# Kernel tuning notes

Hardware: AMD Instinct MI355X
Metric: run time of the kernel (lower is better)

Reference implementation:

```python
import jax, jax.numpy as jnp
import numpy as np

B, N, C = 4, 4096, 1024
H, W = 16, 256
D = C // H  # 64 head_dim


def _rope(t, f):
    # t: (B, N, H, D), f: (N, D//2, 2) -> pairwise rotation on consecutive channel pairs
    tr = t.reshape(*t.shape[:-1], D // 2, 2)
    fc = f.reshape(1, N, 1, D // 2, 2)
    out = jnp.stack([
        tr[..., 0] * fc[..., 0] - tr[..., 1] * fc[..., 1],
        tr[..., 1] * fc[..., 0] + tr[..., 0] * fc[..., 1],
    ], axis=-1)
    return out.reshape(t.shape)


def setup_inputs() -> dict:
    key = jax.random.key(0)
    ks = jax.random.split(key, 4)
    x = jax.random.normal(ks[0], (B, N, C), dtype=jnp.float32)
    freqs_cis = jax.random.normal(ks[1], (N, D // 2, 2), dtype=jnp.float32)
    qkv_w = jax.random.normal(ks[2], (3 * C, C), dtype=jnp.float32) * (C ** -0.5)
    proj_w = jax.random.normal(ks[3], (C, C), dtype=jnp.float32) * (C ** -0.5)
    proj_b = jnp.zeros((C,), dtype=jnp.float32)
    return {"x": x, "freqs_cis": freqs_cis, "qkv_w": qkv_w, "proj_w": proj_w, "proj_b": proj_b}


def reference(x, freqs_cis, qkv_w, proj_w, proj_b):
    nW = N // W
    scale = D ** -0.5
    qkv = (x @ qkv_w.T).reshape(B, N, 3, H, D)
    q, k, v = qkv[:, :, 0], qkv[:, :, 1], qkv[:, :, 2]  # (B, N, H, D)
    q = _rope(q, freqs_cis)
    k = _rope(k, freqs_cis)
    # block-diagonal window attention: q_idx//W == kv_idx//W
    qw = q.transpose(0, 2, 1, 3).reshape(B, H, nW, W, D)
    kw = k.transpose(0, 2, 1, 3).reshape(B, H, nW, W, D)
    vw = v.transpose(0, 2, 1, 3).reshape(B, H, nW, W, D)
    scores = jnp.einsum('bhwqd,bhwkd->bhwqk', qw, kw) * scale
    attn = jax.nn.softmax(scores, axis=-1)
    out = jnp.einsum('bhwqk,bhwkd->bhwqd', attn, vw)
    out = out.reshape(B, H, N, D).transpose(0, 2, 1, 3).reshape(B, N, C)
    return out @ proj_w.T + proj_b
```

## Files before the change

### kernel.cpp

```cpp
#include <hip/hip_runtime.h>
#include <stdint.h>
#include <stddef.h>

typedef __bf16 bf16;
typedef __bf16 bf16x4 __attribute__((ext_vector_type(4)));
typedef __bf16 bf16x8 __attribute__((ext_vector_type(8)));
typedef float f32x4 __attribute__((ext_vector_type(4)));

#define MFMA(a, b, c) __builtin_amdgcn_mfma_f32_16x16x32_bf16(a, b, c, 0, 0, 0)

static constexpr int kB = 4, kN = 4096, kC = 1024, kH = 16, kD = 64;
static constexpr int kM = kB * kN;
static constexpr int kK = 1024;
static constexpr int kQKVN = 3072;

__device__ __forceinline__ void cp16(const void* g, void* l) {
  __builtin_amdgcn_global_load_lds(
      (const __attribute__((address_space(1))) void*)g,
      (__attribute__((address_space(3))) void*)l, 16, 0, 0);
}

__global__ __launch_bounds__(256) void cvt_bf16(const float* __restrict__ src,
                                                bf16* __restrict__ dst, int n4) {
  const int i = blockIdx.x * 256 + threadIdx.x;
  if (i < n4) {
    const float4 v = ((const float4*)src)[i];
    bf16x4 o = {(bf16)v.x, (bf16)v.y, (bf16)v.z, (bf16)v.w};
    *(bf16x4*)&dst[4 * i] = o;
  }
}

__device__ __forceinline__ bf16x8 rope8(bf16x8 t, bf16x8 f) {
  bf16x8 o;
#pragma unroll
  for (int p = 0; p < 4; ++p) {
    float t0 = (float)t[2 * p], t1 = (float)t[2 * p + 1];
    float f0 = (float)f[2 * p], f1 = (float)f[2 * p + 1];
    o[2 * p]     = (bf16)(t0 * f0 - t1 * f1);
    o[2 * p + 1] = (bf16)(t1 * f0 + t0 * f1);
  }
  return o;
}

template <int NOUT, bool BIAS, typename OutT>
__global__ __launch_bounds__(512, 2) void gemm_bt(const bf16* __restrict__ A,
                                                  const bf16* __restrict__ Bw,
                                                  const float* __restrict__ bias,
                                                  OutT* __restrict__ Cout) {
  __shared__ unsigned short As[4][256 * 32];
  __shared__ unsigned short Bs[4][256 * 32];
  const int tid = threadIdx.x;
  const int wave = tid >> 6, lane = tid & 63;
  const int q4 = lane >> 4, l16 = lane & 15;
  const int wr = wave >> 2, wc = wave & 3;

  const int nwg = gridDim.x * gridDim.y;
  int bid = blockIdx.y * gridDim.x + blockIdx.x;
  bid = (bid & 7) * (nwg >> 3) + (bid >> 3);
  const int bx = bid % gridDim.x, by = bid / gridDim.x;
  const int n0 = bx * 256, m0 = by * 256;

  constexpr int NT = kK / 32;

  f32x4 acc[8][4] = {};

  auto stageA = [&](int kt) {
    const int buf = kt & 3;
#pragma unroll
    for (int i = 0; i < 2; ++i) {
      const int c = i * 512 + tid;
      const int row = c >> 2, s = c & 3;
      const int kb = s ^ ((row >> 1) & 3);
      cp16(A + (size_t)(m0 + row) * kK + kt * 32 + kb * 8, &As[buf][c * 8]);
    }
  };
  auto stageB = [&](int kt) {
    const int buf = kt & 3;
#pragma unroll
    for (int i = 0; i < 2; ++i) {
      const int c = i * 512 + tid;
      const int row = c >> 2, s = c & 3;
      const int kb = s ^ ((row >> 1) & 3);
      cp16(Bw + (size_t)(n0 + row) * kK + kt * 32 + kb * 8, &Bs[buf][c * 8]);
    }
  };

  stageA(0); stageB(0); stageA(1); stageB(1); stageA(2); stageB(2);
  asm volatile("s_waitcnt vmcnt(8)\n\ts_barrier" ::: "memory");

  const int slot8 = (q4 ^ ((l16 >> 1) & 3)) * 8;
  const int arow = wr * 128 + l16;
  const int bcol = wc * 64 + l16;

  for (int t = 0; t < NT; ++t) {
    const int rb = t & 3;
    bf16x8 a[8], b0, b1;
#pragma unroll
    for (int i = 0; i < 8; ++i)
      a[i] = *(const bf16x8*)&As[rb][(arow + i * 16) * 32 + slot8];
    b0 = *(const bf16x8*)&Bs[rb][bcol * 32 + slot8];
    b1 = *(const bf16x8*)&Bs[rb][(bcol + 16) * 32 + slot8];
    if (t + 3 < NT) stageA(t + 3);
    if (t < NT - 3)
      asm volatile("s_waitcnt vmcnt(8)\n\ts_barrier" ::: "memory");
    else if (t == NT - 3)
      asm volatile("s_waitcnt vmcnt(6)\n\ts_barrier" ::: "memory");
    else if (t == NT - 2)
      asm volatile("s_waitcnt vmcnt(2)\n\ts_barrier" ::: "memory");
    else
      asm volatile("s_waitcnt vmcnt(0)\n\ts_barrier" ::: "memory");
    __builtin_amdgcn_s_setprio(1);
#pragma unroll
    for (int i = 0; i < 8; ++i) {
      acc[i][0] = MFMA(a[i], b0, acc[i][0]);
      acc[i][1] = MFMA(a[i], b1, acc[i][1]);
    }
    __builtin_amdgcn_s_setprio(0);
    asm volatile("s_barrier" ::: "memory");

    bf16x8 b2 = *(const bf16x8*)&Bs[rb][(bcol + 32) * 32 + slot8];
    bf16x8 b3 = *(const bf16x8*)&Bs[rb][(bcol + 48) * 32 + slot8];
    if (t + 3 < NT) stageB(t + 3);
    if (t < NT - 3)
      asm volatile("s_waitcnt vmcnt(8)\n\ts_barrier" ::: "memory");
    else if (t == NT - 3)
      asm volatile("s_waitcnt vmcnt(4)\n\ts_barrier" ::: "memory");
    else
      asm volatile("s_waitcnt vmcnt(0)\n\ts_barrier" ::: "memory");
    __builtin_amdgcn_s_setprio(1);
#pragma unroll
    for (int i = 0; i < 8; ++i) {
      acc[i][2] = MFMA(a[i], b2, acc[i][2]);
      acc[i][3] = MFMA(a[i], b3, acc[i][3]);
    }
    __builtin_amdgcn_s_setprio(0);
    asm volatile("s_barrier" ::: "memory");
  }

#pragma unroll
  for (int i = 0; i < 8; ++i) {
    const int rowb = m0 + wr * 128 + i * 16 + q4 * 4;
#pragma unroll
    for (int j = 0; j < 4; ++j) {
      const int col = n0 + wc * 64 + j * 16 + l16;
      const float bv = BIAS ? bias[col] : 0.0f;
#pragma unroll
      for (int r = 0; r < 4; ++r)
        Cout[(size_t)(rowb + r) * NOUT + col] = (OutT)(acc[i][j][r] + bv);
    }
  }
}

__global__ __launch_bounds__(256) void attn_win(const bf16* __restrict__ qkv,
                                                const bf16* __restrict__ freqs,
                                                bf16* __restrict__ ob) {
  __shared__ unsigned short k8[8 * 128 * 8];
  __shared__ unsigned short v8[16 * 64 * 8];
  __shared__ unsigned short p8[4 * 16 * 16 * 8];

  const int bid = blockIdx.x;
  const int w = bid & 15, h = (bid >> 4) & 15, b = bid >> 8;
  const int n0 = w * 256;
  const int tid = threadIdx.x;
  const int wave = tid >> 6, lane = tid & 63;
  const int q4 = lane >> 4, l16 = lane & 15;
  const float scale = 0.125f;

  bf16x8 qf[4][2];
#pragma unroll
  for (int g = 0; g < 4; ++g) {
    const int n = n0 + wave * 64 + g * 16 + l16;
    const bf16* qrow = qkv + (size_t)(b * kN + n) * kQKVN + h * kD;
    const bf16* frow = freqs + (size_t)n * kD;
#pragma unroll
    for (int s = 0; s < 2; ++s) {
      const int d0 = s * 32 + q4 * 8;
      qf[g][s] = rope8(*(const bf16x8*)(qrow + d0), *(const bf16x8*)(frow + d0));
    }
  }

  f32x4 O[4][4] = {};
  float mrow[4][4], lrow[4][4];
#pragma unroll
  for (int g = 0; g < 4; ++g)
#pragma unroll
    for (int r = 0; r < 4; ++r) { mrow[g][r] = -3.0e38f; lrow[g][r] = 0.0f; }

  for (int c = 0; c < 2; ++c) {
    const int nc = n0 + c * 128;
    __syncthreads();
#pragma unroll
    for (int i = 0; i < 4; ++i) {
      const int cid = i * 256 + tid;
      const int tok = cid & 127, db = cid >> 7;
      const int n = nc + tok;
      const size_t base = (size_t)(b * kN + n) * kQKVN + h * kD + db * 8;
      bf16x8 kv = *(const bf16x8*)(qkv + base + kC);
      bf16x8 fv = *(const bf16x8*)(freqs + (size_t)n * kD + db * 8);
      *(bf16x8*)&k8[(db * 128 + tok) * 8] = rope8(kv, fv);
      bf16x8 vv = *(const bf16x8*)(qkv + base + 2 * kC);
#pragma unroll
      for (int e = 0; e < 8; ++e)
        ((bf16*)v8)[((tok >> 3) * 64 + db * 8 + e) * 8 + (tok & 7)] = vv[e];
    }
    __syncthreads();

#pragma unroll
    for (int g = 0; g < 4; ++g) {
      f32x4 S[8] = {};
#pragma unroll
      for (int j = 0; j < 8; ++j)
#pragma unroll
        for (int s = 0; s < 2; ++s) {
          bf16x8 kf = *(const bf16x8*)&k8[((q4 + 4 * s) * 128 + j * 16 + l16) * 8];
          S[j] = MFMA(qf[g][s], kf, S[j]);
        }
      float mx[4], sm[4], al[4];
#pragma unroll
      for (int r = 0; r < 4; ++r) {
        float m = -3.0e38f;
#pragma unroll
        for (int j = 0; j < 8; ++j) { S[j][r] *= scale; m = fmaxf(m, S[j][r]); }
        mx[r] = m;
      }
#pragma unroll
      for (int off = 1; off < 16; off <<= 1)
#pragma unroll
        for (int r = 0; r < 4; ++r) mx[r] = fmaxf(mx[r], __shfl_xor(mx[r], off));
#pragma unroll
      for (int r = 0; r < 4; ++r) {
        const float mnew = fmaxf(mrow[g][r], mx[r]);
        al[r] = __expf(mrow[g][r] - mnew);
        mrow[g][r] = mnew;
        sm[r] = 0.0f;
      }
#pragma unroll
      for (int j = 0; j < 8; ++j)
#pragma unroll
        for (int r = 0; r < 4; ++r) {
          const float p = __expf(S[j][r] - mrow[g][r]);
          S[j][r] = p;
          sm[r] += p;
        }
#pragma unroll
      for (int off = 1; off < 16; off <<= 1)
#pragma unroll
        for (int r = 0; r < 4; ++r) sm[r] += __shfl_xor(sm[r], off);
#pragma unroll
      for (int r = 0; r < 4; ++r) lrow[g][r] = lrow[g][r] * al[r] + sm[r];
#pragma unroll
      for (int jd = 0; jd < 4; ++jd)
#pragma unroll
        for (int r = 0; r < 4; ++r) O[g][jd][r] *= al[r];
#pragma unroll
      for (int j = 0; j < 8; ++j) {
        const int tok = j * 16 + l16;
        const int tb = tok >> 3, slot = tok & 7;
#pragma unroll
        for (int r = 0; r < 4; ++r)
          ((bf16*)p8)[((wave * 16 + tb) * 16 + q4 * 4 + r) * 8 + slot] = (bf16)S[j][r];
      }
      asm volatile("s_waitcnt lgkmcnt(0)" ::: "memory");
#pragma unroll
      for (int s4 = 0; s4 < 4; ++s4) {
        bf16x8 pf = *(const bf16x8*)&p8[((wave * 16 + q4 + 4 * s4) * 16 + l16) * 8];
#pragma unroll
        for (int jd = 0; jd < 4; ++jd) {
          bf16x8 vf = *(const bf16x8*)&v8[((q4 + 4 * s4) * 64 + l16 + 16 * jd) * 8];
          O[g][jd] = MFMA(pf, vf, O[g][jd]);
        }
      }
      asm volatile("" ::: "memory");
    }
  }

#pragma unroll
  for (int g = 0; g < 4; ++g) {
    const int nb = n0 + wave * 64 + g * 16 + q4 * 4;
#pragma unroll
    for (int jd = 0; jd < 4; ++jd) {
      const int d = l16 + 16 * jd;
#pragma unroll
      for (int r = 0; r < 4; ++r) {
        const float v = O[g][jd][r] / lrow[g][r];
        ob[(size_t)(b * kN + nb + r) * kC + h * kD + d] = (bf16)v;
      }
    }
  }
}

extern "C" void kernel_launch(void* const* d_in, const int* in_sizes, int n_in,
                              void* d_out, int out_size, void* d_ws, size_t ws_size,
                              hipStream_t stream) {
  (void)in_sizes; (void)n_in; (void)out_size; (void)ws_size;
  const float* x      = (const float*)d_in[0];
  const float* freqs  = (const float*)d_in[1];
  const float* qkv_w  = (const float*)d_in[2];
  const float* proj_w = (const float*)d_in[3];
  const float* proj_b = (const float*)d_in[4];
  float* out = (float*)d_out;

  bf16* qkv_buf = (bf16*)d_ws;
  bf16* shared  = qkv_buf + (size_t)kM * kQKVN;
  bf16* x_b     = shared;
  bf16* attn_b  = shared;
  bf16* qkvw_b  = shared + (size_t)kM * kC;
  bf16* projw_b = qkvw_b + (size_t)kQKVN * kC;
  bf16* freqs_b = projw_b + (size_t)kC * kC;

  cvt_bf16<<<(kM * kC / 4 + 255) / 256, 256, 0, stream>>>(x, x_b, kM * kC / 4);
  cvt_bf16<<<(kQKVN * kC / 4 + 255) / 256, 256, 0, stream>>>(qkv_w, qkvw_b, kQKVN * kC / 4);
  cvt_bf16<<<(kC * kC / 4 + 255) / 256, 256, 0, stream>>>(proj_w, projw_b, kC * kC / 4);
  cvt_bf16<<<(kN * kD / 4 + 255) / 256, 256, 0, stream>>>(freqs, freqs_b, kN * kD / 4);

  gemm_bt<kQKVN, false, bf16><<<dim3(kQKVN / 256, kM / 256), 512, 0, stream>>>(
      x_b, qkvw_b, nullptr, qkv_buf);
  attn_win<<<dim3(kB * kH * (kN / 256)), 256, 0, stream>>>(qkv_buf, freqs_b, attn_b);
  gemm_bt<kC, true, float><<<dim3(kC / 256, kM / 256), 512, 0, stream>>>(
      attn_b, projw_b, proj_b, out);
}
```

Before: 379.2 us.

## Transpose score MFMA, simplify softmax reductions, swizzle P and V LDS layouts

```diff
diff --git a/kernel.cpp b/kernel.cpp
--- a/kernel.cpp
+++ b/kernel.cpp
@@ -156,7 +156,7 @@
                                                 bf16* __restrict__ ob) {
   __shared__ unsigned short k8[8 * 128 * 8];
   __shared__ unsigned short v8[16 * 64 * 8];
-  __shared__ unsigned short p8[4 * 16 * 16 * 8];
+  __shared__ unsigned short pT[4][16 * 128];
 
   const int bid = blockIdx.x;
   const int w = bid & 15, h = (bid >> 4) & 15, b = bid >> 8;
@@ -165,6 +165,8 @@
   const int wave = tid >> 6, lane = tid & 63;
   const int q4 = lane >> 4, l16 = lane & 15;
   const float scale = 0.125f;
+  const int swz = (l16 & 7) << 4;
+  char* const pw = (char*)&pT[wave][0];
 
   bf16x8 qf[4][2];
 #pragma unroll
@@ -180,11 +182,9 @@
   }
 
   f32x4 O[4][4] = {};
-  float mrow[4][4], lrow[4][4];
-#pragma unroll
-  for (int g = 0; g < 4; ++g)
-#pragma unroll
-    for (int r = 0; r < 4; ++r) { mrow[g][r] = -3.0e38f; lrow[g][r] = 0.0f; }
+  float mrow[4], lrow[4];
+#pragma unroll
+  for (int g = 0; g < 4; ++g) { mrow[g] = -3.0e38f; lrow[g] = 0.0f; }
 
   for (int c = 0; c < 2; ++c) {
     const int nc = n0 + c * 128;
@@ -199,9 +199,12 @@
       bf16x8 fv = *(const bf16x8*)(freqs + (size_t)n * kD + db * 8);
       *(bf16x8*)&k8[(db * 128 + tok) * 8] = rope8(kv, fv);
       bf16x8 vv = *(const bf16x8*)(qkv + base + 2 * kC);
-#pragma unroll
-      for (int e = 0; e < 8; ++e)
-        ((bf16*)v8)[((tok >> 3) * 64 + db * 8 + e) * 8 + (tok & 7)] = vv[e];
+      const int tb = tok >> 3, sl = tok & 7;
+#pragma unroll
+      for (int e = 0; e < 8; ++e) {
+        const int d = db * 8 + e;
+        ((bf16*)v8)[((tb * 64) + (d ^ (tb & 7))) * 8 + sl] = vv[e];
+      }
     }
     __syncthreads();
 
@@ -213,60 +216,54 @@
 #pragma unroll
         for (int s = 0; s < 2; ++s) {
           bf16x8 kf = *(const bf16x8*)&k8[((q4 + 4 * s) * 128 + j * 16 + l16) * 8];
-          S[j] = MFMA(qf[g][s], kf, S[j]);
+          S[j] = MFMA(kf, qf[g][s], S[j]);
         }
-      float mx[4], sm[4], al[4];
-#pragma unroll
-      for (int r = 0; r < 4; ++r) {
-        float m = -3.0e38f;
-#pragma unroll
-        for (int j = 0; j < 8; ++j) { S[j][r] *= scale; m = fmaxf(m, S[j][r]); }
-        mx[r] = m;
-      }
-#pragma unroll
-      for (int off = 1; off < 16; off <<= 1)
-#pragma unroll
-        for (int r = 0; r < 4; ++r) mx[r] = fmaxf(mx[r], __shfl_xor(mx[r], off));
-#pragma unroll
-      for (int r = 0; r < 4; ++r) {
-        const float mnew = fmaxf(mrow[g][r], mx[r]);
-        al[r] = __expf(mrow[g][r] - mnew);
-        mrow[g][r] = mnew;
-        sm[r] = 0.0f;
-      }
-#pragma unroll
-      for (int j = 0; j < 8; ++j)
-#pragma unroll
-        for (int r = 0; r < 4; ++r) {
-          const float p = __expf(S[j][r] - mrow[g][r]);
-          S[j][r] = p;
-          sm[r] += p;
-        }
-#pragma unroll
-      for (int off = 1; off < 16; off <<= 1)
-#pragma unroll
-        for (int r = 0; r < 4; ++r) sm[r] += __shfl_xor(sm[r], off);
-#pragma unroll
-      for (int r = 0; r < 4; ++r) lrow[g][r] = lrow[g][r] * al[r] + sm[r];
+      float m0_ = -3.0e38f, m1_ = -3.0e38f, m2_ = -3.0e38f, m3_ = -3.0e38f;
+#pragma unroll
+      for (int j = 0; j < 8; ++j) {
+        S[j][0] *= scale; S[j][1] *= scale; S[j][2] *= scale; S[j][3] *= scale;
+        m0_ = fmaxf(m0_, S[j][0]); m1_ = fmaxf(m1_, S[j][1]);
+        m2_ = fmaxf(m2_, S[j][2]); m3_ = fmaxf(m3_, S[j][3]);
+      }
+      float mx = fmaxf(fmaxf(m0_, m1_), fmaxf(m2_, m3_));
+      mx = fmaxf(mx, __shfl_xor(mx, 16));
+      mx = fmaxf(mx, __shfl_xor(mx, 32));
+      const float mnew = fmaxf(mrow[g], mx);
+      const float al = __expf(mrow[g] - mnew);
+      mrow[g] = mnew;
+      float s0 = 0.f, s1 = 0.f, s2 = 0.f, s3 = 0.f;
+#pragma unroll
+      for (int j = 0; j < 8; ++j) {
+        S[j][0] = __expf(S[j][0] - mnew); s0 += S[j][0];
+        S[j][1] = __expf(S[j][1] - mnew); s1 += S[j][1];
+        S[j][2] = __expf(S[j][2] - mnew); s2 += S[j][2];
+        S[j][3] = __expf(S[j][3] - mnew); s3 += S[j][3];
+      }
+      float sm = (s0 + s1) + (s2 + s3);
+      sm += __shfl_xor(sm, 16);
+      sm += __shfl_xor(sm, 32);
+      lrow[g] = lrow[g] * al + sm;
+      float alr[4];
+#pragma unroll
+      for (int r = 0; r < 4; ++r) alr[r] = __shfl(al, q4 * 4 + r);
 #pragma unroll
       for (int jd = 0; jd < 4; ++jd)
 #pragma unroll
-        for (int r = 0; r < 4; ++r) O[g][jd][r] *= al[r];
+        for (int r = 0; r < 4; ++r) O[g][jd][r] *= alr[r];
 #pragma unroll
       for (int j = 0; j < 8; ++j) {
-        const int tok = j * 16 + l16;
-        const int tb = tok >> 3, slot = tok & 7;
-#pragma unroll
-        for (int r = 0; r < 4; ++r)
-          ((bf16*)p8)[((wave * 16 + tb) * 16 + q4 * 4 + r) * 8 + slot] = (bf16)S[j][r];
+        bf16x4 pk = {(bf16)S[j][0], (bf16)S[j][1], (bf16)S[j][2], (bf16)S[j][3]};
+        *(bf16x4*)(pw + l16 * 256 + ((j * 32 + q4 * 8) ^ swz)) = pk;
       }
       asm volatile("s_waitcnt lgkmcnt(0)" ::: "memory");
 #pragma unroll
       for (int s4 = 0; s4 < 4; ++s4) {
-        bf16x8 pf = *(const bf16x8*)&p8[((wave * 16 + q4 + 4 * s4) * 16 + l16) * 8];
+        bf16x8 pf = *(const bf16x8*)(pw + l16 * 256 + ((s4 * 64 + q4 * 16) ^ swz));
+        const int tb2 = q4 + 4 * s4;
 #pragma unroll
         for (int jd = 0; jd < 4; ++jd) {
-          bf16x8 vf = *(const bf16x8*)&v8[((q4 + 4 * s4) * 64 + l16 + 16 * jd) * 8];
+          const int d2 = (l16 + 16 * jd) ^ (tb2 & 7);
+          bf16x8 vf = *(const bf16x8*)&v8[(tb2 * 64 + d2) * 8];
           O[g][jd] = MFMA(pf, vf, O[g][jd]);
         }
       }
@@ -276,13 +273,16 @@
 
 #pragma unroll
   for (int g = 0; g < 4; ++g) {
+    float lr[4];
+#pragma unroll
+    for (int r = 0; r < 4; ++r) lr[r] = __shfl(lrow[g], q4 * 4 + r);
     const int nb = n0 + wave * 64 + g * 16 + q4 * 4;
 #pragma unroll
     for (int jd = 0; jd < 4; ++jd) {
       const int d = l16 + 16 * jd;
 #pragma unroll
       for (int r = 0; r < 4; ++r) {
-        const float v = O[g][jd][r] / lrow[g][r];
+        const float v = O[g][jd][r] / lr[r];
         ob[(size_t)(b * kN + nb + r) * kC + h * kD + d] = (bf16)v;
       }
     }
```

Measured after the change: 367.4 us. 3.1% less time.
